# Optimization experiments

Hardware: AMD Instinct MI355X
Metric: run time of the kernel (lower is better)

The kernel has to match this reference:

```python
import jax, jax.numpy as jnp
from jax import lax
import numpy as np

B, N = 16, 4096
NPOINTS = [512, 64, 1]
NSAMPLE = [32, 64, 64]
RADIUS = [0.1, 0.2, 0.4]
SA_SPECS = [[9, 64, 128], [131, 128, 256], [259, 512, 1024]]  # use_xyz adds 3 to each input
CLS_SPEC = [1024, 1024, 512, 128]


def _mk(key, shape):
    return jax.random.normal(key, shape, jnp.float32) * 0.05


def setup_inputs() -> dict:
    key = jax.random.key(0)
    ks = iter(jax.random.split(key, 64))
    inp = {"pointcloud": jax.random.uniform(next(ks), (B, N, 9), jnp.float32)}
    # SA shared-MLP layers: 1x1 conv weight + folded eval-mode BN (scale g, bias b)
    for s, spec in enumerate(SA_SPECS):
        for l in range(len(spec) - 1):
            cin, cout = spec[l], spec[l + 1]
            inp[f"sa{s}w{l}"] = _mk(next(ks), (cout, cin))
            inp[f"sa{s}g{l}"] = jnp.ones((cout,), jnp.float32) + _mk(next(ks), (cout,))
            inp[f"sa{s}b{l}"] = _mk(next(ks), (cout,))
    for l in range(3):
        cin, cout = CLS_SPEC[l], CLS_SPEC[l + 1]
        inp[f"clsw{l}"] = _mk(next(ks), (cout, cin))
        inp[f"clsg{l}"] = jnp.ones((cout,), jnp.float32) + _mk(next(ks), (cout,))
        inp[f"clsb{l}"] = _mk(next(ks), (cout,))
    inp["clsw3"] = _mk(next(ks), (63, 128))
    inp["clsb3"] = _mk(next(ks), (63,))
    return inp


def fps(xyz, npoint):
    """Furthest point sampling. xyz: [B,N,3] -> indices [B,npoint]."""
    Bb, Nn, _ = xyz.shape

    def step(carry, _):
        dist, far = carry
        cen = jnp.take_along_axis(xyz, far[:, None, None], axis=1)  # [B,1,3]
        d = jnp.sum((xyz - cen) ** 2, -1)
        dist = jnp.minimum(dist, d)
        return (dist, jnp.argmax(dist, -1).astype(jnp.int32)), far

    init = (jnp.full((Bb, Nn), 1e10, xyz.dtype), jnp.zeros((Bb,), jnp.int32))
    _, idx = lax.scan(step, init, None, length=npoint)
    return jnp.transpose(idx)  # [B, npoint]


def ball_query(radius, K, xyz, new_xyz):
    """First-K-in-index-order neighbors within radius; pad with first hit (0 if none)."""
    Nn = xyz.shape[1]
    d2 = jnp.sum((new_xyz[:, :, None, :] - xyz[:, None, :, :]) ** 2, -1)  # [B,S,N]
    cand = jnp.where(d2 < radius * radius, jnp.arange(Nn, dtype=jnp.int32), Nn)
    vals = -lax.top_k(-cand, K)[0]  # K smallest candidate indices, ascending
    first = vals[..., :1]
    idx = jnp.where(vals >= Nn, first, vals)
    return jnp.where(idx >= Nn, 0, idx)


def sa_module(xyz, feats, npoint, radius, K, layers):
    s_idx = fps(xyz, npoint)
    new_xyz = jnp.take_along_axis(xyz, s_idx[:, :, None], axis=1)  # [B,S,3]
    idx = ball_query(radius, K, xyz, new_xyz)  # [B,S,K]
    gxyz = jax.vmap(lambda p, i: p[i])(xyz, idx) - new_xyz[:, :, None, :]  # [B,S,K,3]
    x = jnp.transpose(gxyz, (0, 3, 1, 2))  # [B,3,S,K]
    gf = jax.vmap(lambda f, i: f[:, i])(feats, idx)  # [B,C,S,K]
    x = jnp.concatenate([x, gf], axis=1)
    for (w, g, b) in layers:  # 1x1 conv + folded BN + ReLU
        x = jax.nn.relu(jnp.einsum('oc,bcsk->bosk', w, x) * g[:, None, None] + b[:, None, None])
    return new_xyz, jnp.max(x, axis=-1)  # max-pool over neighborhood -> [B,Cout,S]


def reference(pointcloud, sa0w0, sa0g0, sa0b0, sa0w1, sa0g1, sa0b1,
              sa1w0, sa1g0, sa1b0, sa1w1, sa1g1, sa1b1,
              sa2w0, sa2g0, sa2b0, sa2w1, sa2g1, sa2b1,
              clsw0, clsg0, clsb0, clsw1, clsg1, clsb1,
              clsw2, clsg2, clsb2, clsw3, clsb3):
    xyz = pointcloud[..., :3]
    feats = jnp.transpose(pointcloud[..., 3:], (0, 2, 1))  # [B,6,N]
    sa_params = [
        [(sa0w0, sa0g0, sa0b0), (sa0w1, sa0g1, sa0b1)],
        [(sa1w0, sa1g0, sa1b0), (sa1w1, sa1g1, sa1b1)],
        [(sa2w0, sa2g0, sa2b0), (sa2w1, sa2g1, sa2b1)],
    ]
    for k in range(3):
        xyz, feats = sa_module(xyz, feats, NPOINTS[k], RADIUS[k], NSAMPLE[k], sa_params[k])
    x = feats  # [B,1024,1]
    for (w, g, b) in [(clsw0, clsg0, clsb0), (clsw1, clsg1, clsb1), (clsw2, clsg2, clsb2)]:
        x = jax.nn.relu(jnp.einsum('oc,bcn->bon', w, x) * g[:, None] + b[:, None])
    return jnp.einsum('oc,bcn->bon', clsw3, x) + clsb3[:, None]  # [B,63,1]
```

## Files before the change

### kernel.cpp

```cpp
#include <hip/hip_runtime.h>

#define DEV __device__ __forceinline__

static constexpr int NB = 16;
static constexpr int N0 = 4096;

DEV float nf_mul(float a, float b){ float r = a*b; asm volatile("" : "+v"(r)); return r; }
DEV float nf_add(float a, float b){ float r = a+b; asm volatile("" : "+v"(r)); return r; }
DEV float d2nf(float dx, float dy, float dz){
  return nf_add(nf_add(nf_mul(dx,dx), nf_mul(dy,dy)), nf_mul(dz,dz));
}

#define DPP_STEP(CTRL) { \
  int hi=(int)(k>>32), lo=(int)k; \
  int ohi=__builtin_amdgcn_update_dpp(hi,hi,CTRL,0xf,0xf,false); \
  int olo=__builtin_amdgcn_update_dpp(lo,lo,CTRL,0xf,0xf,false); \
  unsigned long long ok=((unsigned long long)(unsigned)ohi<<32)|(unsigned)olo; \
  if (ok>k) k=ok; }

DEV unsigned long long dpp_max_key63(unsigned long long k){
  DPP_STEP(0x118)
  DPP_STEP(0x114)
  DPP_STEP(0x112)
  DPP_STEP(0x111)
  DPP_STEP(0x142)
  DPP_STEP(0x143)
  return k;
}

DEV void tr1(int i, const float* __restrict__ in, float* __restrict__ out, int C, int R){
  int r = i / C, c = i - r*C; out[(size_t)c*R + r] = in[i];
}
__global__ __launch_bounds__(256)
void k_prep_all(const float* __restrict__ pc, float4* __restrict__ xyz,
                const float* __restrict__ w00, float* __restrict__ o00,
                const float* __restrict__ w01, float* __restrict__ o01,
                const float* __restrict__ w10, float* __restrict__ o10,
                const float* __restrict__ w11, float* __restrict__ o11,
                const float* __restrict__ w20, float* __restrict__ o20,
                const float* __restrict__ w21, float* __restrict__ o21)
{
  int i = blockIdx.x*256 + threadIdx.x;
  if (i < 65536){
    const float* p = pc + (size_t)i*9;
    xyz[i] = make_float4(p[0], p[1], p[2], 0.f);
    return;
  }
  i -= 65536;
  if (i < 576)    { tr1(i, w00, o00, 9, 64);     return; } i -= 576;
  if (i < 8192)   { tr1(i, w01, o01, 64, 128);   return; } i -= 8192;
  if (i < 16768)  { tr1(i, w10, o10, 131, 128);  return; } i -= 16768;
  if (i < 32768)  { tr1(i, w11, o11, 128, 256);  return; } i -= 32768;
  if (i < 132608) { tr1(i, w20, o20, 259, 512);  return; } i -= 132608;
  if (i < 524288) { tr1(i, w21, o21, 512, 1024); return; }
}

template<int N, int NP, int NT, int NP2>
__global__ __launch_bounds__(NT)
void k_fps2(const float4* __restrict__ xyz, float4* __restrict__ nx, float4* __restrict__ nx2)
{
  constexpr int PT = N / NT;
  constexpr int NW = NT / 64;
  constexpr int PT2 = NP / NT;
  __shared__ float sx[N], sy[N], sz[N];
  __shared__ float c1x[NP], c1y[NP], c1z[NP];
  __shared__ unsigned long long exch[2][NW];
  const int b = blockIdx.x, t = threadIdx.x, w = t >> 6, lane = t & 63;
  const float4* xb = xyz + (size_t)b*N;
  float px[PT], py[PT], pz[PT], pd[PT];
  #pragma unroll
  for (int j=0;j<PT;j++){
    int i = t + j*NT;
    float4 v = xb[i];
    px[j]=v.x; py[j]=v.y; pz[j]=v.z; pd[j]=1e10f;
    sx[i]=v.x; sy[i]=v.y; sz[i]=v.z;
  }
  __syncthreads();
  float cx = sx[0], cy = sy[0], cz = sz[0];
  for (int it=0; it<NP; it++){
    if (t==0){
      nx[(size_t)b*NP + it] = make_float4(cx,cy,cz,0.f);
      c1x[it]=cx; c1y[it]=cy; c1z[it]=cz;
    }
    unsigned long long best = 0;
    #pragma unroll
    for (int j=0;j<PT;j++){
      float d = d2nf(px[j]-cx, py[j]-cy, pz[j]-cz);
      pd[j] = fminf(pd[j], d);
      unsigned long long k = ((unsigned long long)__float_as_uint(pd[j])<<32)
                           | (unsigned)~(t + j*NT);
      if (k > best) best = k;
    }
    { unsigned long long k = best; DPP_STEP(0x118) DPP_STEP(0x114) DPP_STEP(0x112)
      DPP_STEP(0x111) DPP_STEP(0x142) DPP_STEP(0x143) best = k; }
    if (lane == 63) exch[it&1][w] = best;
    __syncthreads();
    unsigned long long g = exch[it&1][0];
    #pragma unroll
    for (int k2=1;k2<NW;k2++){ unsigned long long e = exch[it&1][k2]; if (e > g) g = e; }
    int far = (int)~(unsigned)g;
    cx = sx[far]; cy = sy[far]; cz = sz[far];
  }
  if constexpr (NP2 > 0){
    float qx[PT2], qy[PT2], qz[PT2], qd[PT2];
    #pragma unroll
    for (int j=0;j<PT2;j++){
      int i = t + j*NT;
      qx[j]=c1x[i]; qy[j]=c1y[i]; qz[j]=c1z[i]; qd[j]=1e10f;
    }
    float ax = c1x[0], ay = c1y[0], az = c1z[0];
    for (int it=0; it<NP2; it++){
      if (t==0) nx2[(size_t)b*NP2 + it] = make_float4(ax,ay,az,0.f);
      unsigned long long best = 0;
      #pragma unroll
      for (int j=0;j<PT2;j++){
        float d = d2nf(qx[j]-ax, qy[j]-ay, qz[j]-az);
        qd[j] = fminf(qd[j], d);
        unsigned long long k = ((unsigned long long)__float_as_uint(qd[j])<<32)
                             | (unsigned)~(t + j*NT);
        if (k > best) best = k;
      }
      { unsigned long long k = best; DPP_STEP(0x118) DPP_STEP(0x114) DPP_STEP(0x112)
        DPP_STEP(0x111) DPP_STEP(0x142) DPP_STEP(0x143) best = k; }
      if (lane == 63) exch[it&1][w] = best;
      __syncthreads();
      unsigned long long g = exch[it&1][0];
      #pragma unroll
      for (int k2=1;k2<NW;k2++){ unsigned long long e = exch[it&1][k2]; if (e > g) g = e; }
      int far = (int)~(unsigned)g;
      ax = c1x[far]; ay = c1y[far]; az = c1z[far];
    }
  }
}

template<int N, int K>
__global__ __launch_bounds__(256)
void k_bq(const float4* __restrict__ xyz, const float4* __restrict__ ctr,
          int* __restrict__ out, int S, int cstride, float r2, int nwav)
{
  int wid = blockIdx.x*4 + (threadIdx.x >> 6);
  if (wid >= nwav) return;
  int lane = threadIdx.x & 63;
  int b = wid / S, s = wid - b*S;
  const float4* xb = xyz + (size_t)b*N;
  float4 c = ctr[(size_t)b*cstride + s];
  int* o = out + ((size_t)b*S + s)*K;
  int cnt = 0, first = 0;
  bool have_first = false;
  for (int base = 0; base < N; base += 64){
    float4 p = xb[base + lane];
    float d = d2nf(p.x - c.x, p.y - c.y, p.z - c.z);
    bool hit = (d <= r2);
    unsigned long long m = __ballot(hit);
    if (m){
      if (!have_first){ first = base + __ffsll((unsigned long long)m) - 1; have_first = true; }
      if (hit){
        int pos = cnt + __popcll(m & ((1ull << lane) - 1ull));
        if (pos < K) o[pos] = base + lane;
      }
      cnt += __popcll(m);
      if (cnt >= K) break;
    }
  }
  for (int pos = cnt + lane; pos < K; pos += 64) o[pos] = first;
}

__global__ __launch_bounds__(256)
void k_sa0(const float4* __restrict__ xyz, const float4* __restrict__ nx0,
           const int* __restrict__ idx0, const float* __restrict__ pc,
           const float* __restrict__ w0tg, const float* __restrict__ g0g, const float* __restrict__ b0g,
           const float* __restrict__ w1tg, const float* __restrict__ g1g, const float* __restrict__ b1g,
           float* __restrict__ f1)
{
  constexpr int K = 32, S = 512, C0 = 64, C1 = 128, G = 8;
  __shared__ float w1t[C0*C1];
  __shared__ float w0t[9*C0];
  __shared__ float gb0[2*C0];
  __shared__ float gb1[2*C1];
  __shared__ float xs[9][K];
  __shared__ float y0[C0][K];
  int t = threadIdx.x;
  for (int i=t;i<C0*C1;i+=256) w1t[i] = w1tg[i];
  for (int i=t;i<9*C0;i+=256)  w0t[i] = w0tg[i];
  if (t < C0){ gb0[t]=g0g[t]; gb0[C0+t]=b0g[t]; }
  if (t < C1){ gb1[t]=g1g[t]; gb1[C1+t]=b1g[t]; }
  int k0 = (t & 7)*4, og = t >> 3;
  for (int gi=0; gi<G; gi++){
    int gid = blockIdx.x*G + gi;
    int b = gid >> 9, s = gid & 511;
    __syncthreads();
    if (t < K){
      int i = idx0[(size_t)gid*K + t];
      float4 cen = nx0[(size_t)b*S + s];
      float4 p = xyz[(size_t)b*N0 + i];
      xs[0][t]=p.x-cen.x; xs[1][t]=p.y-cen.y; xs[2][t]=p.z-cen.z;
      const float* pr = pc + ((size_t)b*N0 + i)*9 + 3;
      #pragma unroll
      for (int f=0;f<6;f++) xs[3+f][t] = pr[f];
    }
    __syncthreads();
    float a0[2][4] = {};
    #pragma unroll
    for (int c=0;c<9;c++){
      float4 xv = *(const float4*)&xs[c][k0];
      #pragma unroll
      for (int j=0;j<2;j++){
        float w = w0t[c*C0 + og*2 + j];
        a0[j][0]+=w*xv.x; a0[j][1]+=w*xv.y; a0[j][2]+=w*xv.z; a0[j][3]+=w*xv.w;
      }
    }
    #pragma unroll
    for (int j=0;j<2;j++){
      int o = og*2 + j;
      float g = gb0[o], bb = gb0[C0+o];
      float4 r;
      r.x=fmaxf(a0[j][0]*g+bb,0.f); r.y=fmaxf(a0[j][1]*g+bb,0.f);
      r.z=fmaxf(a0[j][2]*g+bb,0.f); r.w=fmaxf(a0[j][3]*g+bb,0.f);
      *(float4*)&y0[o][k0] = r;
    }
    __syncthreads();
    float a1[4][4] = {};
    #pragma unroll 4
    for (int c=0;c<C0;c++){
      float4 yv = *(const float4*)&y0[c][k0];
      const float* wp = &w1t[c*C1 + og*4];
      #pragma unroll
      for (int j=0;j<4;j++){
        float w = wp[j];
        a1[j][0]+=w*yv.x; a1[j][1]+=w*yv.y; a1[j][2]+=w*yv.z; a1[j][3]+=w*yv.w;
      }
    }
    #pragma unroll
    for (int j=0;j<4;j++){
      int o = og*4 + j;
      float g = gb1[o], bb = gb1[C1+o];
      float m = fmaxf(fmaxf(a1[j][0]*g+bb, a1[j][1]*g+bb), fmaxf(a1[j][2]*g+bb, a1[j][3]*g+bb));
      m = fmaxf(m, 0.f);
      #pragma unroll
      for (int off=1; off<8; off<<=1) m = fmaxf(m, __shfl_xor(m, off));
      if ((t & 7) == 0) f1[((size_t)b*C1 + o)*S + s] = m;
    }
  }
}

__global__ __launch_bounds__(256)
void k_z1(const float* __restrict__ f1, const float* __restrict__ w0t, float* __restrict__ Z1)
{
  int b = blockIdx.z;
  int obase = blockIdx.x*64, ibase = blockIdx.y*64;
  int t = threadIdx.x;
  int i0 = ibase + (t & 15)*4, ol = (t >> 4)*4;
  float acc[4][4] = {};
  #pragma unroll 4
  for (int c=0;c<128;c++){
    float4 fv = *(const float4*)&f1[((size_t)b*128 + c)*512 + i0];
    float4 wv = *(const float4*)&w0t[(size_t)(3+c)*128 + obase + ol];
    float wa[4] = {wv.x, wv.y, wv.z, wv.w};
    float fa[4] = {fv.x, fv.y, fv.z, fv.w};
    #pragma unroll
    for (int j=0;j<4;j++)
      #pragma unroll
      for (int i=0;i<4;i++) acc[j][i] += wa[j]*fa[i];
  }
  #pragma unroll
  for (int j=0;j<4;j++)
    *(float4*)&Z1[((size_t)b*128 + obase + ol + j)*512 + i0] =
        make_float4(acc[j][0], acc[j][1], acc[j][2], acc[j][3]);
}

__global__ __launch_bounds__(256)
void k_sa1(const float4* __restrict__ nx0, const float4* __restrict__ nx1,
           const int* __restrict__ idx1, const float* __restrict__ Z1,
           const float* __restrict__ w0t, const float* __restrict__ g0, const float* __restrict__ b0,
           const float* __restrict__ w1t, const float* __restrict__ g1, const float* __restrict__ b1,
           float* __restrict__ f2)
{
  constexpr int K = 64, S = 64, C0 = 128, C1 = 256;
  __shared__ float y0[C0][K];
  __shared__ float gx[3][K];
  __shared__ int sidx[K];
  int gid = blockIdx.x, b = gid >> 6, s = gid & 63;
  int t = threadIdx.x;
  if (t < K) sidx[t] = idx1[(size_t)gid*K + t];
  __syncthreads();
  if (t < K){
    float4 cen = nx1[(size_t)b*S + s];
    float4 p = nx0[(size_t)b*512 + sidx[t]];
    gx[0][t]=p.x-cen.x; gx[1][t]=p.y-cen.y; gx[2][t]=p.z-cen.z;
  }
  __syncthreads();
  int k0 = (t & 15)*4, og = t >> 4;
  {
    float4 x0 = *(const float4*)&gx[0][k0];
    float4 x1 = *(const float4*)&gx[1][k0];
    float4 x2 = *(const float4*)&gx[2][k0];
    int i0=sidx[k0], i1=sidx[k0+1], i2=sidx[k0+2], i3=sidx[k0+3];
    #pragma unroll
    for (int j=0;j<8;j++){
      int o = og*8 + j;
      const float* zr = Z1 + ((size_t)b*C0 + o)*512;
      float wx=w0t[o], wy=w0t[C0+o], wz=w0t[2*C0+o];
      float g=g0[o], bb=b0[o];
      float4 r;
      r.x = fmaxf((zr[i0] + wx*x0.x + wy*x1.x + wz*x2.x)*g + bb, 0.f);
      r.y = fmaxf((zr[i1] + wx*x0.y + wy*x1.y + wz*x2.y)*g + bb, 0.f);
      r.z = fmaxf((zr[i2] + wx*x0.z + wy*x1.z + wz*x2.z)*g + bb, 0.f);
      r.w = fmaxf((zr[i3] + wx*x0.w + wy*x1.w + wz*x2.w)*g + bb, 0.f);
      *(float4*)&y0[o][k0] = r;
    }
  }
  __syncthreads();
  float a1[16][4] = {};
  #pragma unroll 2
  for (int c=0;c<C0;c++){
    float4 yv = *(const float4*)&y0[c][k0];
    const float* wp = &w1t[(size_t)c*C1 + og*16];
    #pragma unroll
    for (int j=0;j<16;j++){
      float w = wp[j];
      a1[j][0]+=w*yv.x; a1[j][1]+=w*yv.y; a1[j][2]+=w*yv.z; a1[j][3]+=w*yv.w;
    }
  }
  #pragma unroll
  for (int j=0;j<16;j++){
    int o = og*16 + j;
    float g=g1[o], bb=b1[o];
    float m = fmaxf(fmaxf(a1[j][0]*g+bb, a1[j][1]*g+bb), fmaxf(a1[j][2]*g+bb, a1[j][3]*g+bb));
    m = fmaxf(m, 0.f);
    #pragma unroll
    for (int off=1; off<16; off<<=1) m = fmaxf(m, __shfl_xor(m, off));
    if ((t & 15) == 0) f2[((size_t)b*C1 + o)*S + s] = m;
  }
}

__global__ __launch_bounds__(256)
void k_gather2(const float4* __restrict__ nx1, const int* __restrict__ idx2,
               const float* __restrict__ f2, float* __restrict__ x2)
{
  int b = blockIdx.x, t = threadIdx.x;
  __shared__ int sidx[64];
  if (t < 64) sidx[t] = idx2[b*64 + t];
  __syncthreads();
  float4 cen = nx1[(size_t)b*64];
  float* xo = x2 + (size_t)b*259*64;
  if (t < 64){
    float4 p = nx1[(size_t)b*64 + sidx[t]];
    xo[t] = p.x - cen.x; xo[64 + t] = p.y - cen.y; xo[128 + t] = p.z - cen.z;
  }
  for (int i=t; i<256*64; i+=256){
    int c = i >> 6, k = i & 63;
    xo[(3+c)*64 + k] = f2[((size_t)b*256 + c)*64 + sidx[k]];
  }
}

__global__ __launch_bounds__(256)
void k_sa2_l0(const float* __restrict__ x2, const float* __restrict__ w0t,
              const float* __restrict__ g0, const float* __restrict__ b0,
              float* __restrict__ y2)
{
  int b = blockIdx.y;
  int obase = blockIdx.x*64;
  int t = threadIdx.x;
  int k0 = (t & 15)*4, ol = (t >> 4)*4;
  const float* xb = x2 + (size_t)b*259*64;
  float acc[4][4] = {};
  #pragma unroll 4
  for (int c=0;c<259;c++){
    float4 xv = *(const float4*)&xb[c*64 + k0];
    float4 wv = *(const float4*)&w0t[(size_t)c*512 + obase + ol];
    float wa[4] = {wv.x, wv.y, wv.z, wv.w};
    float xa[4] = {xv.x, xv.y, xv.z, xv.w};
    #pragma unroll
    for (int j=0;j<4;j++)
      #pragma unroll
      for (int i=0;i<4;i++) acc[j][i] += wa[j]*xa[i];
  }
  #pragma unroll
  for (int j=0;j<4;j++){
    int o = obase + ol + j;
    float g = g0[o], bb = b0[o];
    float4 r;
    r.x=fmaxf(acc[j][0]*g+bb,0.f); r.y=fmaxf(acc[j][1]*g+bb,0.f);
    r.z=fmaxf(acc[j][2]*g+bb,0.f); r.w=fmaxf(acc[j][3]*g+bb,0.f);
    *(float4*)&y2[((size_t)b*512 + o)*64 + k0] = r;
  }
}

__global__ __launch_bounds__(256)
void k_sa2_l1(const float* __restrict__ y2, const float* __restrict__ w1t,
              const float* __restrict__ g1, const float* __restrict__ b1,
              float* __restrict__ f3)
{
  int b = blockIdx.y;
  int obase = blockIdx.x*64;
  int t = threadIdx.x;
  int k0 = (t & 15)*4, ol = (t >> 4)*4;
  const float* yb = y2 + (size_t)b*512*64;
  float acc[4][4] = {};
  #pragma unroll 4
  for (int c=0;c<512;c++){
    float4 yv = *(const float4*)&yb[c*64 + k0];
    float4 wv = *(const float4*)&w1t[(size_t)c*1024 + obase + ol];
    float wa[4] = {wv.x, wv.y, wv.z, wv.w};
    float ya[4] = {yv.x, yv.y, yv.z, yv.w};
    #pragma unroll
    for (int j=0;j<4;j++)
      #pragma unroll
      for (int i=0;i<4;i++) acc[j][i] += wa[j]*ya[i];
  }
  #pragma unroll
  for (int j=0;j<4;j++){
    int o = obase + ol + j;
    float g = g1[o], bb = b1[o];
    float m = fmaxf(fmaxf(acc[j][0]*g+bb, acc[j][1]*g+bb), fmaxf(acc[j][2]*g+bb, acc[j][3]*g+bb));
    m = fmaxf(m, 0.f);
    #pragma unroll
    for (int off=1; off<16; off<<=1) m = fmaxf(m, __shfl_xor(m, off));
    if ((t & 15) == 0) f3[(size_t)b*1024 + o] = m;
  }
}

template<bool RELU>
__global__ __launch_bounds__(256)
void k_lin(const float* __restrict__ x, const float* __restrict__ w,
           const float* __restrict__ g, const float* __restrict__ bb,
           float* __restrict__ y, int Cin, int Cout)
{
  __shared__ float xs[1024];
  int b = blockIdx.y, t = threadIdx.x;
  const float* xb = x + (size_t)b*Cin;
  for (int i=t;i<Cin;i+=256) xs[i] = xb[i];
  __syncthreads();
  int o = blockIdx.x*256 + t;
  if (o < Cout){
    const float4* wr = (const float4*)(w + (size_t)o*Cin);
    float acc = 0.f;
    #pragma unroll 8
    for (int c=0;c<Cin/4;c++){
      float4 wv = wr[c]; float4 xv = *(const float4*)&xs[c*4];
      acc += wv.x*xv.x + wv.y*xv.y + wv.z*xv.z + wv.w*xv.w;
    }
    float r;
    if (RELU) r = fmaxf(acc*g[o] + bb[o], 0.f);
    else      r = acc + bb[o];
    y[(size_t)b*Cout + o] = r;
  }
}

extern "C" void kernel_launch(void* const* d_in, const int* in_sizes, int n_in,
                              void* d_out, int out_size, void* d_ws, size_t ws_size,
                              hipStream_t stream)
{
  (void)in_sizes; (void)n_in; (void)out_size; (void)ws_size;
  const float* pc    = (const float*)d_in[0];
  const float* sa0w0 = (const float*)d_in[1];
  const float* sa0g0 = (const float*)d_in[2];
  const float* sa0b0 = (const float*)d_in[3];
  const float* sa0w1 = (const float*)d_in[4];
  const float* sa0g1 = (const float*)d_in[5];
  const float* sa0b1 = (const float*)d_in[6];
  const float* sa1w0 = (const float*)d_in[7];
  const float* sa1g0 = (const float*)d_in[8];
  const float* sa1b0 = (const float*)d_in[9];
  const float* sa1w1 = (const float*)d_in[10];
  const float* sa1g1 = (const float*)d_in[11];
  const float* sa1b1 = (const float*)d_in[12];
  const float* sa2w0 = (const float*)d_in[13];
  const float* sa2g0 = (const float*)d_in[14];
  const float* sa2b0 = (const float*)d_in[15];
  const float* sa2w1 = (const float*)d_in[16];
  const float* sa2g1 = (const float*)d_in[17];
  const float* sa2b1 = (const float*)d_in[18];
  const float* clsw0 = (const float*)d_in[19];
  const float* clsg0 = (const float*)d_in[20];
  const float* clsb0 = (const float*)d_in[21];
  const float* clsw1 = (const float*)d_in[22];
  const float* clsg1 = (const float*)d_in[23];
  const float* clsb1 = (const float*)d_in[24];
  const float* clsw2 = (const float*)d_in[25];
  const float* clsg2 = (const float*)d_in[26];
  const float* clsb2 = (const float*)d_in[27];
  const float* clsw3 = (const float*)d_in[28];
  const float* clsb3 = (const float*)d_in[29];

  char* ws = (char*)d_ws;
  size_t off = 0;
  auto A = [&](size_t bytes)->char* {
    char* p = ws + off;
    off = (off + bytes + 255) & ~(size_t)255;
    return p;
  };
  float4* xyz0 = (float4*)A((size_t)NB*N0*16);
  float4* nx0  = (float4*)A((size_t)NB*512*16);
  float4* nx1  = (float4*)A((size_t)NB*64*16);
  int*   idx0  = (int*)  A((size_t)NB*512*32*4);
  int*   idx1  = (int*)  A((size_t)NB*64*64*4);
  int*   idx2  = (int*)  A((size_t)NB*64*4);
  float* f1    = (float*)A((size_t)NB*128*512*4);
  float* Z1    = (float*)A((size_t)NB*128*512*4);
  float* f2    = (float*)A((size_t)NB*256*64*4);
  float* x2    = (float*)A((size_t)NB*259*64*4);
  float* y2    = (float*)A((size_t)NB*512*64*4);
  float* f3    = (float*)A((size_t)NB*1024*4);
  float* cb0   = (float*)A((size_t)NB*1024*4);
  float* cb1   = (float*)A((size_t)NB*512*4);
  float* cb2   = (float*)A((size_t)NB*128*4);
  float* w0t0  = (float*)A((size_t)9*64*4);
  float* w1t0  = (float*)A((size_t)64*128*4);
  float* w0t1  = (float*)A((size_t)131*128*4);
  float* w1t1  = (float*)A((size_t)128*256*4);
  float* w0t2  = (float*)A((size_t)259*512*4);
  float* w1t2  = (float*)A((size_t)512*1024*4);

  k_prep_all<<<(780736 + 255)/256, 256, 0, stream>>>(pc, xyz0,
      sa0w0, w0t0, sa0w1, w1t0, sa1w0, w0t1, sa1w1, w1t1, sa2w0, w0t2, sa2w1, w1t2);

  k_fps2<4096, 512, 256, 64><<<NB, 256, 0, stream>>>(xyz0, nx0, nx1);

  k_bq<4096, 32><<<(NB*512 + 3)/4, 256, 0, stream>>>(xyz0, nx0, idx0, 512, 512, 0.01f, NB*512);
  k_sa0<<<(NB*512)/8, 256, 0, stream>>>(xyz0, nx0, idx0, pc,
                                        w0t0, sa0g0, sa0b0, w1t0, sa0g1, sa0b1, f1);
  k_bq<512, 64><<<(NB*64 + 3)/4, 256, 0, stream>>>(nx0, nx1, idx1, 64, 64, 0.04f, NB*64);
  k_z1<<<dim3(2, 8, NB), 256, 0, stream>>>(f1, w0t1, Z1);
  k_sa1<<<NB*64, 256, 0, stream>>>(nx0, nx1, idx1, Z1,
                                   w0t1, sa1g0, sa1b0, w1t1, sa1g1, sa1b1, f2);
  k_bq<64, 64><<<(NB + 3)/4, 256, 0, stream>>>(nx1, nx1, idx2, 1, 64, 0.16f, NB);
  k_gather2<<<NB, 256, 0, stream>>>(nx1, idx2, f2, x2);
  k_sa2_l0<<<dim3(8, NB), 256, 0, stream>>>(x2, w0t2, sa2g0, sa2b0, y2);
  k_sa2_l1<<<dim3(16, NB), 256, 0, stream>>>(y2, w1t2, sa2g1, sa2b1, f3);
  k_lin<true ><<<dim3(4, NB), 256, 0, stream>>>(f3,  clsw0, clsg0, clsb0, cb0, 1024, 1024);
  k_lin<true ><<<dim3(2, NB), 256, 0, stream>>>(cb0, clsw1, clsg1, clsb1, cb1, 1024, 512);
  k_lin<true ><<<dim3(1, NB), 256, 0, stream>>>(cb1, clsw2, clsg2, clsb2, cb2, 512, 128);
  k_lin<false><<<dim3(1, NB), 256, 0, stream>>>(cb2, clsw3, clsb3, clsb3, (float*)d_out, 128, 63);
}
```

Baseline: 877.9 us.

## Fuse prep with FPS, merge ball queries, pack FPS distance math

Prep and furthest-point sampling now run in one launch: the first 16 blocks run FPS reading the point cloud directly, and the remaining blocks do the xyz/weight transposes. The three ball-query launches become one kernel that dispatches by wave index. Inside FPS, distance math uses packed v_pk f32 ops on point pairs. The 64-bit key argmax is replaced by a float max reduction followed by an int min over the tied indices. This cuts launch count and the serial per-iteration latency of FPS. The cost is two DPP reductions plus a readlane per iteration, and packed-math rounding that may differ from the old non-fused order.

```diff
diff --git a/kernel.cpp b/kernel.cpp
--- a/kernel.cpp
+++ b/kernel.cpp
@@ -4,6 +4,8 @@
 
 static constexpr int NB = 16;
 static constexpr int N0 = 4096;
+
+typedef float v2f __attribute__((ext_vector_type(2)));
 
 DEV float nf_mul(float a, float b){ float r = a*b; asm volatile("" : "+v"(r)); return r; }
 DEV float nf_add(float a, float b){ float r = a+b; asm volatile("" : "+v"(r)); return r; }
@@ -11,140 +13,164 @@
   return nf_add(nf_add(nf_mul(dx,dx), nf_mul(dy,dy)), nf_mul(dz,dz));
 }
 
-#define DPP_STEP(CTRL) { \
-  int hi=(int)(k>>32), lo=(int)k; \
-  int ohi=__builtin_amdgcn_update_dpp(hi,hi,CTRL,0xf,0xf,false); \
-  int olo=__builtin_amdgcn_update_dpp(lo,lo,CTRL,0xf,0xf,false); \
-  unsigned long long ok=((unsigned long long)(unsigned)ohi<<32)|(unsigned)olo; \
-  if (ok>k) k=ok; }
-
-DEV unsigned long long dpp_max_key63(unsigned long long k){
-  DPP_STEP(0x118)
-  DPP_STEP(0x114)
-  DPP_STEP(0x112)
-  DPP_STEP(0x111)
-  DPP_STEP(0x142)
-  DPP_STEP(0x143)
-  return k;
+DEV v2f pk_sub(v2f a, v2f b){ v2f r; asm("v_pk_add_f32 %0, %1, %2 neg_lo:[0,1] neg_hi:[0,1]" : "=v"(r) : "v"(a), "v"(b)); return r; }
+DEV v2f pk_mul(v2f a, v2f b){ v2f r; asm("v_pk_mul_f32 %0, %1, %2" : "=v"(r) : "v"(a), "v"(b)); return r; }
+DEV v2f pk_add(v2f a, v2f b){ v2f r; asm("v_pk_add_f32 %0, %1, %2" : "=v"(r) : "v"(a), "v"(b)); return r; }
+DEV v2f d2pk(v2f dx, v2f dy, v2f dz){
+  return pk_add(pk_add(pk_mul(dx,dx), pk_mul(dy,dy)), pk_mul(dz,dz));
+}
+
+DEV float dpp_max63(float v){
+  int o;
+  o = __builtin_amdgcn_update_dpp(__float_as_int(v), __float_as_int(v), 0x118, 0xf, 0xf, false); v = fmaxf(v, __int_as_float(o));
+  o = __builtin_amdgcn_update_dpp(__float_as_int(v), __float_as_int(v), 0x114, 0xf, 0xf, false); v = fmaxf(v, __int_as_float(o));
+  o = __builtin_amdgcn_update_dpp(__float_as_int(v), __float_as_int(v), 0x112, 0xf, 0xf, false); v = fmaxf(v, __int_as_float(o));
+  o = __builtin_amdgcn_update_dpp(__float_as_int(v), __float_as_int(v), 0x111, 0xf, 0xf, false); v = fmaxf(v, __int_as_float(o));
+  o = __builtin_amdgcn_update_dpp(__float_as_int(v), __float_as_int(v), 0x142, 0xf, 0xf, false); v = fmaxf(v, __int_as_float(o));
+  o = __builtin_amdgcn_update_dpp(__float_as_int(v), __float_as_int(v), 0x143, 0xf, 0xf, false); v = fmaxf(v, __int_as_float(o));
+  return v;
+}
+DEV int dpp_min63(int v){
+  int o;
+  o = __builtin_amdgcn_update_dpp(v, v, 0x118, 0xf, 0xf, false); v = min(v, o);
+  o = __builtin_amdgcn_update_dpp(v, v, 0x114, 0xf, 0xf, false); v = min(v, o);
+  o = __builtin_amdgcn_update_dpp(v, v, 0x112, 0xf, 0xf, false); v = min(v, o);
+  o = __builtin_amdgcn_update_dpp(v, v, 0x111, 0xf, 0xf, false); v = min(v, o);
+  o = __builtin_amdgcn_update_dpp(v, v, 0x142, 0xf, 0xf, false); v = min(v, o);
+  o = __builtin_amdgcn_update_dpp(v, v, 0x143, 0xf, 0xf, false); v = min(v, o);
+  return v;
 }
 
 DEV void tr1(int i, const float* __restrict__ in, float* __restrict__ out, int C, int R){
   int r = i / C, c = i - r*C; out[(size_t)c*R + r] = in[i];
 }
-__global__ __launch_bounds__(256)
-void k_prep_all(const float* __restrict__ pc, float4* __restrict__ xyz,
-                const float* __restrict__ w00, float* __restrict__ o00,
-                const float* __restrict__ w01, float* __restrict__ o01,
-                const float* __restrict__ w10, float* __restrict__ o10,
-                const float* __restrict__ w11, float* __restrict__ o11,
-                const float* __restrict__ w20, float* __restrict__ o20,
-                const float* __restrict__ w21, float* __restrict__ o21)
-{
-  int i = blockIdx.x*256 + threadIdx.x;
-  if (i < 65536){
-    const float* p = pc + (size_t)i*9;
-    xyz[i] = make_float4(p[0], p[1], p[2], 0.f);
+
+__global__ __launch_bounds__(256)
+void k_front(const float* __restrict__ pc, float4* __restrict__ xyz,
+             float4* __restrict__ nx0, float4* __restrict__ nx1,
+             const float* __restrict__ w00, float* __restrict__ o00,
+             const float* __restrict__ w01, float* __restrict__ o01,
+             const float* __restrict__ w10, float* __restrict__ o10,
+             const float* __restrict__ w11, float* __restrict__ o11,
+             const float* __restrict__ w20, float* __restrict__ o20,
+             const float* __restrict__ w21, float* __restrict__ o21)
+{
+  constexpr int N = 4096, NP = 512, NT = 256, NP2 = 64, NW = NT/64, NPR = N/(2*NT);
+  if (blockIdx.x >= NB){
+    int i = (int)(blockIdx.x - NB)*256 + threadIdx.x;
+    if (i < 65536){
+      const float* p = pc + (size_t)i*9;
+      xyz[i] = make_float4(p[0], p[1], p[2], 0.f);
+      return;
+    }
+    i -= 65536;
+    if (i < 576)    { tr1(i, w00, o00, 9, 64);     return; } i -= 576;
+    if (i < 8192)   { tr1(i, w01, o01, 64, 128);   return; } i -= 8192;
+    if (i < 16768)  { tr1(i, w10, o10, 131, 128);  return; } i -= 16768;
+    if (i < 32768)  { tr1(i, w11, o11, 128, 256);  return; } i -= 32768;
+    if (i < 132608) { tr1(i, w20, o20, 259, 512);  return; } i -= 132608;
+    if (i < 524288) { tr1(i, w21, o21, 512, 1024); return; }
     return;
   }
-  i -= 65536;
-  if (i < 576)    { tr1(i, w00, o00, 9, 64);     return; } i -= 576;
-  if (i < 8192)   { tr1(i, w01, o01, 64, 128);   return; } i -= 8192;
-  if (i < 16768)  { tr1(i, w10, o10, 131, 128);  return; } i -= 16768;
-  if (i < 32768)  { tr1(i, w11, o11, 128, 256);  return; } i -= 32768;
-  if (i < 132608) { tr1(i, w20, o20, 259, 512);  return; } i -= 132608;
-  if (i < 524288) { tr1(i, w21, o21, 512, 1024); return; }
-}
-
-template<int N, int NP, int NT, int NP2>
-__global__ __launch_bounds__(NT)
-void k_fps2(const float4* __restrict__ xyz, float4* __restrict__ nx, float4* __restrict__ nx2)
-{
-  constexpr int PT = N / NT;
-  constexpr int NW = NT / 64;
-  constexpr int PT2 = NP / NT;
   __shared__ float sx[N], sy[N], sz[N];
-  __shared__ float c1x[NP], c1y[NP], c1z[NP];
+  __shared__ float4 c1p[NP];
   __shared__ unsigned long long exch[2][NW];
-  const int b = blockIdx.x, t = threadIdx.x, w = t >> 6, lane = t & 63;
-  const float4* xb = xyz + (size_t)b*N;
-  float px[PT], py[PT], pz[PT], pd[PT];
+  const int b = blockIdx.x, t = threadIdx.x, lane = t & 63, w = t >> 6;
+  const float* src = pc + (size_t)b*N*9;
+  v2f px[NPR], py[NPR], pz[NPR], pd[NPR];
   #pragma unroll
-  for (int j=0;j<PT;j++){
-    int i = t + j*NT;
-    float4 v = xb[i];
-    px[j]=v.x; py[j]=v.y; pz[j]=v.z; pd[j]=1e10f;
-    sx[i]=v.x; sy[i]=v.y; sz[i]=v.z;
+  for (int p=0;p<NPR;p++){
+    int i0 = t + (2*p)*NT, i1 = i0 + NT;
+    const float* a0 = src + (size_t)i0*9;
+    const float* a1 = src + (size_t)i1*9;
+    float x0=a0[0], y0=a0[1], z0=a0[2], x1=a1[0], y1=a1[1], z1=a1[2];
+    v2f vx = {x0,x1}, vy = {y0,y1}, vz = {z0,z1}, vd = {1e10f,1e10f};
+    px[p]=vx; py[p]=vy; pz[p]=vz; pd[p]=vd;
+    sx[i0]=x0; sy[i0]=y0; sz[i0]=z0;
+    sx[i1]=x1; sy[i1]=y1; sz[i1]=z1;
   }
   __syncthreads();
   float cx = sx[0], cy = sy[0], cz = sz[0];
   for (int it=0; it<NP; it++){
     if (t==0){
-      nx[(size_t)b*NP + it] = make_float4(cx,cy,cz,0.f);
-      c1x[it]=cx; c1y[it]=cy; c1z[it]=cz;
-    }
-    unsigned long long best = 0;
-    #pragma unroll
-    for (int j=0;j<PT;j++){
-      float d = d2nf(px[j]-cx, py[j]-cy, pz[j]-cz);
-      pd[j] = fminf(pd[j], d);
-      unsigned long long k = ((unsigned long long)__float_as_uint(pd[j])<<32)
-                           | (unsigned)~(t + j*NT);
-      if (k > best) best = k;
-    }
-    { unsigned long long k = best; DPP_STEP(0x118) DPP_STEP(0x114) DPP_STEP(0x112)
-      DPP_STEP(0x111) DPP_STEP(0x142) DPP_STEP(0x143) best = k; }
-    if (lane == 63) exch[it&1][w] = best;
+      nx0[(size_t)b*NP + it] = make_float4(cx,cy,cz,0.f);
+      c1p[it] = make_float4(cx,cy,cz,0.f);
+    }
+    v2f cx2 = {cx,cx}, cy2 = {cy,cy}, cz2 = {cz,cz};
+    float bv = -1.f; int bi = 0;
+    #pragma unroll
+    for (int p=0;p<NPR;p++){
+      v2f d = d2pk(pk_sub(px[p],cx2), pk_sub(py[p],cy2), pk_sub(pz[p],cz2));
+      float nx_ = fminf(pd[p].x, d.x);
+      float ny_ = fminf(pd[p].y, d.y);
+      pd[p].x = nx_; pd[p].y = ny_;
+      if (nx_ > bv){ bv = nx_; bi = t + (2*p)*NT; }
+      if (ny_ > bv){ bv = ny_; bi = t + (2*p+1)*NT; }
+    }
+    float gmv = dpp_max63(bv);
+    float gm = __int_as_float(__builtin_amdgcn_readlane(__float_as_int(gmv), 63));
+    int cand = (bv == gm) ? bi : 0x7fffffff;
+    cand = dpp_min63(cand);
+    if (lane == 63)
+      exch[it&1][w] = ((unsigned long long)__float_as_uint(gm) << 32) | (unsigned)~cand;
     __syncthreads();
     unsigned long long g = exch[it&1][0];
     #pragma unroll
-    for (int k2=1;k2<NW;k2++){ unsigned long long e = exch[it&1][k2]; if (e > g) g = e; }
+    for (int k=1;k<NW;k++){ unsigned long long e = exch[it&1][k]; if (e > g) g = e; }
     int far = (int)~(unsigned)g;
     cx = sx[far]; cy = sy[far]; cz = sz[far];
   }
-  if constexpr (NP2 > 0){
-    float qx[PT2], qy[PT2], qz[PT2], qd[PT2];
-    #pragma unroll
-    for (int j=0;j<PT2;j++){
-      int i = t + j*NT;
-      qx[j]=c1x[i]; qy[j]=c1y[i]; qz[j]=c1z[i]; qd[j]=1e10f;
-    }
-    float ax = c1x[0], ay = c1y[0], az = c1z[0];
+  {
+    float4 p0 = c1p[t], p1 = c1p[t + NT];
+    v2f qx = {p0.x, p1.x}, qy = {p0.y, p1.y}, qz = {p0.z, p1.z}, qd = {1e10f, 1e10f};
+    float4 a = c1p[0];
     for (int it=0; it<NP2; it++){
-      if (t==0) nx2[(size_t)b*NP2 + it] = make_float4(ax,ay,az,0.f);
-      unsigned long long best = 0;
-      #pragma unroll
-      for (int j=0;j<PT2;j++){
-        float d = d2nf(qx[j]-ax, qy[j]-ay, qz[j]-az);
-        qd[j] = fminf(qd[j], d);
-        unsigned long long k = ((unsigned long long)__float_as_uint(qd[j])<<32)
-                             | (unsigned)~(t + j*NT);
-        if (k > best) best = k;
-      }
-      { unsigned long long k = best; DPP_STEP(0x118) DPP_STEP(0x114) DPP_STEP(0x112)
-        DPP_STEP(0x111) DPP_STEP(0x142) DPP_STEP(0x143) best = k; }
-      if (lane == 63) exch[it&1][w] = best;
+      if (t==0) nx1[(size_t)b*NP2 + it] = make_float4(a.x,a.y,a.z,0.f);
+      v2f ax2 = {a.x,a.x}, ay2 = {a.y,a.y}, az2 = {a.z,a.z};
+      v2f d = d2pk(pk_sub(qx,ax2), pk_sub(qy,ay2), pk_sub(qz,az2));
+      float nx_ = fminf(qd.x, d.x);
+      float ny_ = fminf(qd.y, d.y);
+      qd.x = nx_; qd.y = ny_;
+      float bv = nx_; int bi = t;
+      if (ny_ > bv){ bv = ny_; bi = t + NT; }
+      float gmv = dpp_max63(bv);
+      float gm = __int_as_float(__builtin_amdgcn_readlane(__float_as_int(gmv), 63));
+      int cand = (bv == gm) ? bi : 0x7fffffff;
+      cand = dpp_min63(cand);
+      if (lane == 63)
+        exch[it&1][w] = ((unsigned long long)__float_as_uint(gm) << 32) | (unsigned)~cand;
       __syncthreads();
       unsigned long long g = exch[it&1][0];
       #pragma unroll
-      for (int k2=1;k2<NW;k2++){ unsigned long long e = exch[it&1][k2]; if (e > g) g = e; }
+      for (int k=1;k<NW;k++){ unsigned long long e = exch[it&1][k]; if (e > g) g = e; }
       int far = (int)~(unsigned)g;
-      ax = c1x[far]; ay = c1y[far]; az = c1z[far];
-    }
-  }
-}
-
-template<int N, int K>
-__global__ __launch_bounds__(256)
-void k_bq(const float4* __restrict__ xyz, const float4* __restrict__ ctr,
-          int* __restrict__ out, int S, int cstride, float r2, int nwav)
+      float4 af = c1p[far];
+      a = af;
+    }
+  }
+}
+
+__global__ __launch_bounds__(256)
+void k_bq_all(const float4* __restrict__ xyz0, const float4* __restrict__ nx0,
+              const float4* __restrict__ nx1,
+              int* __restrict__ idx0, int* __restrict__ idx1, int* __restrict__ idx2)
 {
   int wid = blockIdx.x*4 + (threadIdx.x >> 6);
-  if (wid >= nwav) return;
   int lane = threadIdx.x & 63;
-  int b = wid / S, s = wid - b*S;
-  const float4* xb = xyz + (size_t)b*N;
-  float4 c = ctr[(size_t)b*cstride + s];
-  int* o = out + ((size_t)b*S + s)*K;
+  const float4* xb; float4 c; int* o; int N, K; float r2;
+  if (wid < 8192){
+    int b = wid >> 9, s = wid & 511;
+    xb = xyz0 + (size_t)b*4096; c = nx0[(size_t)b*512 + s];
+    o = idx0 + ((size_t)b*512 + s)*32; N = 4096; K = 32; r2 = 0.01f;
+  } else if (wid < 9216){
+    int u = wid - 8192; int b = u >> 6, s = u & 63;
+    xb = nx0 + (size_t)b*512; c = nx1[(size_t)b*64 + s];
+    o = idx1 + ((size_t)b*64 + s)*64; N = 512; K = 64; r2 = 0.04f;
+  } else {
+    int b = wid - 9216;
+    xb = nx1 + (size_t)b*64; c = nx1[(size_t)b*64];
+    o = idx2 + (size_t)b*64; N = 64; K = 64; r2 = 0.16f;
+  }
   int cnt = 0, first = 0;
   bool have_first = false;
   for (int base = 0; base < N; base += 64){
@@ -512,19 +538,16 @@
   float* w0t2  = (float*)A((size_t)259*512*4);
   float* w1t2  = (float*)A((size_t)512*1024*4);
 
-  k_prep_all<<<(780736 + 255)/256, 256, 0, stream>>>(pc, xyz0,
+  k_front<<<NB + 3050, 256, 0, stream>>>(pc, xyz0, nx0, nx1,
       sa0w0, w0t0, sa0w1, w1t0, sa1w0, w0t1, sa1w1, w1t1, sa2w0, w0t2, sa2w1, w1t2);
 
-  k_fps2<4096, 512, 256, 64><<<NB, 256, 0, stream>>>(xyz0, nx0, nx1);
-
-  k_bq<4096, 32><<<(NB*512 + 3)/4, 256, 0, stream>>>(xyz0, nx0, idx0, 512, 512, 0.01f, NB*512);
+  k_bq_all<<<2308, 256, 0, stream>>>(xyz0, nx0, nx1, idx0, idx1, idx2);
+
   k_sa0<<<(NB*512)/8, 256, 0, stream>>>(xyz0, nx0, idx0, pc,
                                         w0t0, sa0g0, sa0b0, w1t0, sa0g1, sa0b1, f1);
-  k_bq<512, 64><<<(NB*64 + 3)/4, 256, 0, stream>>>(nx0, nx1, idx1, 64, 64, 0.04f, NB*64);
   k_z1<<<dim3(2, 8, NB), 256, 0, stream>>>(f1, w0t1, Z1);
   k_sa1<<<NB*64, 256, 0, stream>>>(nx0, nx1, idx1, Z1,
                                    w0t1, sa1g0, sa1b0, w1t1, sa1g1, sa1b1, f2);
-  k_bq<64, 64><<<(NB + 3)/4, 256, 0, stream>>>(nx1, nx1, idx2, 1, 64, 0.16f, NB);
   k_gather2<<<NB, 256, 0, stream>>>(nx1, idx2, f2, x2);
   k_sa2_l0<<<dim3(8, NB), 256, 0, stream>>>(x2, w0t2, sa2g0, sa2b0, y2);
   k_sa2_l1<<<dim3(16, NB), 256, 0, stream>>>(y2, w1t2, sa2g1, sa2b1, f3);
```

Measured after the change: 861.2 us. About the same (-1.9%).

## Fuse prep with FPS and merge three ball-query launches into one

Applied to the files above, without the earlier changes.

The prep kernel and the FPS kernel become one launch: the first NB blocks run FPS, reading xyz straight from the pointcloud, while the remaining blocks do the xyz repacking and weight transposes concurrently. The three ball-query launches are merged into a single kernel that picks its level from the wave index. FPS shared storage moves to float4 arrays so a centre is fetched with one load, and the inline-asm no-fusion distance helper becomes a contract(off) expression. The aim is to remove launch gaps and the serial prep-to-FPS dependency; the cost is that FPS blocks, which dominate runtime, now share the GPU with prep blocks.

```diff
diff --git a/kernel.cpp b/kernel.cpp
--- a/kernel.cpp
+++ b/kernel.cpp
@@ -5,10 +5,9 @@
 static constexpr int NB = 16;
 static constexpr int N0 = 4096;
 
-DEV float nf_mul(float a, float b){ float r = a*b; asm volatile("" : "+v"(r)); return r; }
-DEV float nf_add(float a, float b){ float r = a+b; asm volatile("" : "+v"(r)); return r; }
-DEV float d2nf(float dx, float dy, float dz){
-  return nf_add(nf_add(nf_mul(dx,dx), nf_mul(dy,dy)), nf_mul(dz,dz));
+DEV float d2c(float dx, float dy, float dz){
+#pragma clang fp contract(off)
+  return dx*dx + dy*dy + dz*dz;
 }
 
 #define DPP_STEP(CTRL) { \
@@ -31,64 +30,64 @@
 DEV void tr1(int i, const float* __restrict__ in, float* __restrict__ out, int C, int R){
   int r = i / C, c = i - r*C; out[(size_t)c*R + r] = in[i];
 }
-__global__ __launch_bounds__(256)
-void k_prep_all(const float* __restrict__ pc, float4* __restrict__ xyz,
-                const float* __restrict__ w00, float* __restrict__ o00,
-                const float* __restrict__ w01, float* __restrict__ o01,
-                const float* __restrict__ w10, float* __restrict__ o10,
-                const float* __restrict__ w11, float* __restrict__ o11,
-                const float* __restrict__ w20, float* __restrict__ o20,
-                const float* __restrict__ w21, float* __restrict__ o21)
-{
-  int i = blockIdx.x*256 + threadIdx.x;
-  if (i < 65536){
-    const float* p = pc + (size_t)i*9;
-    xyz[i] = make_float4(p[0], p[1], p[2], 0.f);
+
+__global__ __launch_bounds__(256)
+void k_front(const float* __restrict__ pc, float4* __restrict__ xyz,
+             float4* __restrict__ nx0, float4* __restrict__ nx1,
+             const float* __restrict__ w00, float* __restrict__ o00,
+             const float* __restrict__ w01, float* __restrict__ o01,
+             const float* __restrict__ w10, float* __restrict__ o10,
+             const float* __restrict__ w11, float* __restrict__ o11,
+             const float* __restrict__ w20, float* __restrict__ o20,
+             const float* __restrict__ w21, float* __restrict__ o21)
+{
+  constexpr int N = 4096, NP = 512, NT = 256, NP2 = 64, NW = NT/64, PT = N/NT;
+  if (blockIdx.x >= NB){
+    int i = (int)(blockIdx.x - NB)*256 + threadIdx.x;
+    if (i < 65536){
+      const float* p = pc + (size_t)i*9;
+      xyz[i] = make_float4(p[0], p[1], p[2], 0.f);
+      return;
+    }
+    i -= 65536;
+    if (i < 576)    { tr1(i, w00, o00, 9, 64);     return; } i -= 576;
+    if (i < 8192)   { tr1(i, w01, o01, 64, 128);   return; } i -= 8192;
+    if (i < 16768)  { tr1(i, w10, o10, 131, 128);  return; } i -= 16768;
+    if (i < 32768)  { tr1(i, w11, o11, 128, 256);  return; } i -= 32768;
+    if (i < 132608) { tr1(i, w20, o20, 259, 512);  return; } i -= 132608;
+    if (i < 524288) { tr1(i, w21, o21, 512, 1024); return; }
     return;
   }
-  i -= 65536;
-  if (i < 576)    { tr1(i, w00, o00, 9, 64);     return; } i -= 576;
-  if (i < 8192)   { tr1(i, w01, o01, 64, 128);   return; } i -= 8192;
-  if (i < 16768)  { tr1(i, w10, o10, 131, 128);  return; } i -= 16768;
-  if (i < 32768)  { tr1(i, w11, o11, 128, 256);  return; } i -= 32768;
-  if (i < 132608) { tr1(i, w20, o20, 259, 512);  return; } i -= 132608;
-  if (i < 524288) { tr1(i, w21, o21, 512, 1024); return; }
-}
-
-template<int N, int NP, int NT, int NP2>
-__global__ __launch_bounds__(NT)
-void k_fps2(const float4* __restrict__ xyz, float4* __restrict__ nx, float4* __restrict__ nx2)
-{
-  constexpr int PT = N / NT;
-  constexpr int NW = NT / 64;
-  constexpr int PT2 = NP / NT;
-  __shared__ float sx[N], sy[N], sz[N];
-  __shared__ float c1x[NP], c1y[NP], c1z[NP];
+  __shared__ float4 sp[N];
+  __shared__ float4 c1p[NP];
   __shared__ unsigned long long exch[2][NW];
-  const int b = blockIdx.x, t = threadIdx.x, w = t >> 6, lane = t & 63;
-  const float4* xb = xyz + (size_t)b*N;
+  const int b = blockIdx.x, t = threadIdx.x, lane = t & 63, w = t >> 6;
+  const float* src = pc + (size_t)b*N*9;
   float px[PT], py[PT], pz[PT], pd[PT];
+  unsigned nlo[PT];
   #pragma unroll
   for (int j=0;j<PT;j++){
     int i = t + j*NT;
-    float4 v = xb[i];
-    px[j]=v.x; py[j]=v.y; pz[j]=v.z; pd[j]=1e10f;
-    sx[i]=v.x; sy[i]=v.y; sz[i]=v.z;
+    const float* a = src + (size_t)i*9;
+    float x=a[0], y=a[1], z=a[2];
+    px[j]=x; py[j]=y; pz[j]=z; pd[j]=1e10f;
+    nlo[j] = ~(unsigned)i;
+    sp[i] = make_float4(x,y,z,0.f);
   }
   __syncthreads();
-  float cx = sx[0], cy = sy[0], cz = sz[0];
+  float cx = sp[0].x, cy = sp[0].y, cz = sp[0].z;
   for (int it=0; it<NP; it++){
     if (t==0){
-      nx[(size_t)b*NP + it] = make_float4(cx,cy,cz,0.f);
-      c1x[it]=cx; c1y[it]=cy; c1z[it]=cz;
+      nx0[(size_t)b*NP + it] = make_float4(cx,cy,cz,0.f);
+      c1p[it] = make_float4(cx,cy,cz,0.f);
     }
     unsigned long long best = 0;
     #pragma unroll
     for (int j=0;j<PT;j++){
-      float d = d2nf(px[j]-cx, py[j]-cy, pz[j]-cz);
-      pd[j] = fminf(pd[j], d);
-      unsigned long long k = ((unsigned long long)__float_as_uint(pd[j])<<32)
-                           | (unsigned)~(t + j*NT);
+      float d = d2c(px[j]-cx, py[j]-cy, pz[j]-cz);
+      float nd = fminf(pd[j], d);
+      pd[j] = nd;
+      unsigned long long k = ((unsigned long long)__float_as_uint(nd)<<32) | nlo[j];
       if (k > best) best = k;
     }
     { unsigned long long k = best; DPP_STEP(0x118) DPP_STEP(0x114) DPP_STEP(0x112)
@@ -97,59 +96,65 @@
     __syncthreads();
     unsigned long long g = exch[it&1][0];
     #pragma unroll
-    for (int k2=1;k2<NW;k2++){ unsigned long long e = exch[it&1][k2]; if (e > g) g = e; }
+    for (int q=1;q<NW;q++){ unsigned long long e = exch[it&1][q]; if (e > g) g = e; }
     int far = (int)~(unsigned)g;
-    cx = sx[far]; cy = sy[far]; cz = sz[far];
-  }
-  if constexpr (NP2 > 0){
-    float qx[PT2], qy[PT2], qz[PT2], qd[PT2];
-    #pragma unroll
-    for (int j=0;j<PT2;j++){
-      int i = t + j*NT;
-      qx[j]=c1x[i]; qy[j]=c1y[i]; qz[j]=c1z[i]; qd[j]=1e10f;
-    }
-    float ax = c1x[0], ay = c1y[0], az = c1z[0];
+    float4 c = sp[far];
+    cx = c.x; cy = c.y; cz = c.z;
+  }
+  {
+    float4 p0 = c1p[t], p1 = c1p[t + NT];
+    float qd0 = 1e10f, qd1 = 1e10f;
+    unsigned nl0 = ~(unsigned)t, nl1 = ~(unsigned)(t + NT);
+    float ax = c1p[0].x, ay = c1p[0].y, az = c1p[0].z;
     for (int it=0; it<NP2; it++){
-      if (t==0) nx2[(size_t)b*NP2 + it] = make_float4(ax,ay,az,0.f);
-      unsigned long long best = 0;
-      #pragma unroll
-      for (int j=0;j<PT2;j++){
-        float d = d2nf(qx[j]-ax, qy[j]-ay, qz[j]-az);
-        qd[j] = fminf(qd[j], d);
-        unsigned long long k = ((unsigned long long)__float_as_uint(qd[j])<<32)
-                             | (unsigned)~(t + j*NT);
-        if (k > best) best = k;
-      }
+      if (t==0) nx1[(size_t)b*NP2 + it] = make_float4(ax,ay,az,0.f);
+      float d0 = d2c(p0.x-ax, p0.y-ay, p0.z-az);
+      float d1 = d2c(p1.x-ax, p1.y-ay, p1.z-az);
+      qd0 = fminf(qd0, d0);
+      qd1 = fminf(qd1, d1);
+      unsigned long long best = ((unsigned long long)__float_as_uint(qd0)<<32) | nl0;
+      unsigned long long k1   = ((unsigned long long)__float_as_uint(qd1)<<32) | nl1;
+      if (k1 > best) best = k1;
       { unsigned long long k = best; DPP_STEP(0x118) DPP_STEP(0x114) DPP_STEP(0x112)
         DPP_STEP(0x111) DPP_STEP(0x142) DPP_STEP(0x143) best = k; }
       if (lane == 63) exch[it&1][w] = best;
       __syncthreads();
       unsigned long long g = exch[it&1][0];
       #pragma unroll
-      for (int k2=1;k2<NW;k2++){ unsigned long long e = exch[it&1][k2]; if (e > g) g = e; }
+      for (int q=1;q<NW;q++){ unsigned long long e = exch[it&1][q]; if (e > g) g = e; }
       int far = (int)~(unsigned)g;
-      ax = c1x[far]; ay = c1y[far]; az = c1z[far];
-    }
-  }
-}
-
-template<int N, int K>
-__global__ __launch_bounds__(256)
-void k_bq(const float4* __restrict__ xyz, const float4* __restrict__ ctr,
-          int* __restrict__ out, int S, int cstride, float r2, int nwav)
+      float4 c = c1p[far];
+      ax = c.x; ay = c.y; az = c.z;
+    }
+  }
+}
+
+__global__ __launch_bounds__(256)
+void k_bq_all(const float4* __restrict__ xyz0, const float4* __restrict__ nx0,
+              const float4* __restrict__ nx1,
+              int* __restrict__ idx0, int* __restrict__ idx1, int* __restrict__ idx2)
 {
   int wid = blockIdx.x*4 + (threadIdx.x >> 6);
-  if (wid >= nwav) return;
   int lane = threadIdx.x & 63;
-  int b = wid / S, s = wid - b*S;
-  const float4* xb = xyz + (size_t)b*N;
-  float4 c = ctr[(size_t)b*cstride + s];
-  int* o = out + ((size_t)b*S + s)*K;
+  const float4* xb; float4 c; int* o; int N, K; float r2;
+  if (wid < 8192){
+    int b = wid >> 9, s = wid & 511;
+    xb = xyz0 + (size_t)b*4096; c = nx0[(size_t)b*512 + s];
+    o = idx0 + ((size_t)b*512 + s)*32; N = 4096; K = 32; r2 = 0.01f;
+  } else if (wid < 9216){
+    int u = wid - 8192; int b = u >> 6, s = u & 63;
+    xb = nx0 + (size_t)b*512; c = nx1[(size_t)b*64 + s];
+    o = idx1 + ((size_t)b*64 + s)*64; N = 512; K = 64; r2 = 0.04f;
+  } else {
+    int b = wid - 9216;
+    xb = nx1 + (size_t)b*64; c = nx1[(size_t)b*64];
+    o = idx2 + (size_t)b*64; N = 64; K = 64; r2 = 0.16f;
+  }
   int cnt = 0, first = 0;
   bool have_first = false;
   for (int base = 0; base < N; base += 64){
     float4 p = xb[base + lane];
-    float d = d2nf(p.x - c.x, p.y - c.y, p.z - c.z);
+    float d = d2c(p.x - c.x, p.y - c.y, p.z - c.z);
     bool hit = (d <= r2);
     unsigned long long m = __ballot(hit);
     if (m){
@@ -512,19 +517,16 @@
   float* w0t2  = (float*)A((size_t)259*512*4);
   float* w1t2  = (float*)A((size_t)512*1024*4);
 
-  k_prep_all<<<(780736 + 255)/256, 256, 0, stream>>>(pc, xyz0,
+  k_front<<<NB + 3050, 256, 0, stream>>>(pc, xyz0, nx0, nx1,
       sa0w0, w0t0, sa0w1, w1t0, sa1w0, w0t1, sa1w1, w1t1, sa2w0, w0t2, sa2w1, w1t2);
 
-  k_fps2<4096, 512, 256, 64><<<NB, 256, 0, stream>>>(xyz0, nx0, nx1);
-
-  k_bq<4096, 32><<<(NB*512 + 3)/4, 256, 0, stream>>>(xyz0, nx0, idx0, 512, 512, 0.01f, NB*512);
+  k_bq_all<<<2308, 256, 0, stream>>>(xyz0, nx0, nx1, idx0, idx1, idx2);
+
   k_sa0<<<(NB*512)/8, 256, 0, stream>>>(xyz0, nx0, idx0, pc,
                                         w0t0, sa0g0, sa0b0, w1t0, sa0g1, sa0b1, f1);
-  k_bq<512, 64><<<(NB*64 + 3)/4, 256, 0, stream>>>(nx0, nx1, idx1, 64, 64, 0.04f, NB*64);
   k_z1<<<dim3(2, 8, NB), 256, 0, stream>>>(f1, w0t1, Z1);
   k_sa1<<<NB*64, 256, 0, stream>>>(nx0, nx1, idx1, Z1,
                                    w0t1, sa1g0, sa1b0, w1t1, sa1g1, sa1b1, f2);
-  k_bq<64, 64><<<(NB + 3)/4, 256, 0, stream>>>(nx1, nx1, idx2, 1, 64, 0.16f, NB);
   k_gather2<<<NB, 256, 0, stream>>>(nx1, idx2, f2, x2);
   k_sa2_l0<<<dim3(8, NB), 256, 0, stream>>>(x2, w0t2, sa2g0, sa2b0, y2);
   k_sa2_l1<<<dim3(16, NB), 256, 0, stream>>>(y2, w1t2, sa2g1, sa2b1, f3);
```

Result: faster. 833.0 us (-5.1%).
